# Optimization experiments

Hardware: AMD Instinct MI355X
Metric: run time of the kernel (lower is better)

Reference implementation:

```python
import jax, jax.numpy as jnp
import numpy as np

S, B, E, H = 2048, 2, 1024, 16
DH = E // H
SCALING = DH ** -0.5


def setup_inputs() -> dict:
    key = jax.random.key(0)
    ks = jax.random.split(key, 9)
    std = 1.0 / np.sqrt(E)
    return {
        "query": jax.random.normal(ks[0], (S, B, E), jnp.float32),
        "wq": jax.random.normal(ks[1], (E, E), jnp.float32) * std,
        "bq": jax.random.normal(ks[2], (E,), jnp.float32) * 0.02,
        "wk": jax.random.normal(ks[3], (E, E), jnp.float32) * std,
        "bk": jax.random.normal(ks[4], (E,), jnp.float32) * 0.02,
        "wv": jax.random.normal(ks[5], (E, E), jnp.float32) * std,
        "bv": jax.random.normal(ks[6], (E,), jnp.float32) * 0.02,
        "wo": jax.random.normal(ks[7], (E, E), jnp.float32) * std,
        "bo": jax.random.normal(ks[8], (E,), jnp.float32) * 0.02,
    }


def reference(query, wq, bq, wk, bk, wv, bv, wo, bo):
    # query: [S, B, E] (time, batch, channel), self-attention: key=value=query
    q = (query @ wq.T + bq) * SCALING          # fairseq scales q, not scores
    k = query @ wk.T + bk
    v = query @ wv.T + bv
    # split heads: [S, B, H, DH]
    q = q.reshape(S, B, H, DH)
    k = k.reshape(S, B, H, DH)
    v = v.reshape(S, B, H, DH)
    scores = jnp.einsum("qbhd,kbhd->bhqk", q, k)   # [B, H, S, S]
    probs = jax.nn.softmax(scores, axis=-1)
    ctx = jnp.einsum("bhqk,kbhd->qbhd", probs, v)  # [S, B, H, DH]
    ctx = ctx.reshape(S, B, E)
    return ctx @ wo.T + bo                          # [S, B, E]
```

## Files before the change

kernel.cpp:

```cpp
#include <hip/hip_runtime.h>
#include <hip/hip_bf16.h>
#include <stdint.h>

#define S_LEN 2048
#define BATCH 2
#define EMB   1024
#define NH    16
#define DHEAD 64
#define ROWS  (S_LEN*BATCH)
#define SCALE_Q 0.125f

typedef __attribute__((ext_vector_type(8))) short bf16x8;
typedef __attribute__((ext_vector_type(4))) float f32x4;

typedef const __attribute__((address_space(1))) void* gas_ptr;
typedef __attribute__((address_space(3))) void* las_ptr;
#define GLD16(g, l) __builtin_amdgcn_global_load_lds((gas_ptr)(g), (las_ptr)(l), 16, 0, 0)

__device__ __forceinline__ unsigned short f2b(float f) {
  union { float f; unsigned int u; } v; v.f = f;
  unsigned int u = v.u;
  unsigned int r = (u + 0x7FFFu + ((u >> 16) & 1u)) >> 16;
  return (unsigned short)r;
}

__device__ __forceinline__ void cvt8(const float* __restrict__ s,
                                     unsigned short* __restrict__ d, size_t i) {
  float4 a = *reinterpret_cast<const float4*>(s + i);
  float4 b = *reinterpret_cast<const float4*>(s + i + 4);
  uint4 o;
  o.x = (unsigned)f2b(a.x) | ((unsigned)f2b(a.y) << 16);
  o.y = (unsigned)f2b(a.z) | ((unsigned)f2b(a.w) << 16);
  o.z = (unsigned)f2b(b.x) | ((unsigned)f2b(b.y) << 16);
  o.w = (unsigned)f2b(b.z) | ((unsigned)f2b(b.w) << 16);
  *reinterpret_cast<uint4*>(d + i) = o;
}

__global__ __launch_bounds__(256) void cvt_kernel(const float* __restrict__ s,
                                                  unsigned short* __restrict__ d) {
  size_t i = ((size_t)blockIdx.x * 256 + threadIdx.x) * 8;
  cvt8(s, d, i);
}

__global__ __launch_bounds__(256) void cvt4_kernel(
    const float* __restrict__ s0, const float* __restrict__ s1,
    const float* __restrict__ s2, const float* __restrict__ s3,
    unsigned short* __restrict__ d0, unsigned short* __restrict__ d1,
    unsigned short* __restrict__ d2, unsigned short* __restrict__ d3) {
  const float* s; unsigned short* d;
  switch (blockIdx.y) {
    case 0:  s = s0; d = d0; break;
    case 1:  s = s1; d = d1; break;
    case 2:  s = s2; d = d2; break;
    default: s = s3; d = d3; break;
  }
  size_t i = ((size_t)blockIdx.x * 256 + threadIdx.x) * 8;
  cvt8(s, d, i);
}

__device__ __forceinline__ void gemm_mainloop(const unsigned short* __restrict__ A,
                                              const unsigned short* __restrict__ Bw,
                                              int m0, int n0, f32x4 acc[4][4]) {
  __shared__ unsigned short Abuf[128 * 32];
  __shared__ unsigned short Bbuf[128 * 32];
  const int t    = threadIdx.x;
  const int lane = t & 63;
  const int w    = t >> 6;
  const int wr   = w >> 1, wc = w & 1;
  const int lm   = lane & 15;
  const int lkb  = (lane >> 4) * 8;

  f32x4 zf = {0.0f, 0.0f, 0.0f, 0.0f};
#pragma unroll
  for (int i = 0; i < 4; ++i)
#pragma unroll
    for (int j = 0; j < 4; ++j) acc[i][j] = zf;

  for (int k0 = 0; k0 < EMB; k0 += 32) {
#pragma unroll
    for (int q = 0; q < 2; ++q) {
      int c = t + q * 256;
      int r = c >> 2, ci = c & 3;
      GLD16(A  + (size_t)(m0 + r) * EMB + k0 + ci * 8,
            (char*)Abuf + (size_t)(q * 256 + w * 64) * 16);
      GLD16(Bw + (size_t)(n0 + r) * EMB + k0 + ci * 8,
            (char*)Bbuf + (size_t)(q * 256 + w * 64) * 16);
    }
    __syncthreads();

    bf16x8 af[4], bfr[4];
#pragma unroll
    for (int i = 0; i < 4; ++i)
      af[i] = *reinterpret_cast<const bf16x8*>(&Abuf[(wr * 64 + i * 16 + lm) * 32 + lkb]);
#pragma unroll
    for (int j = 0; j < 4; ++j)
      bfr[j] = *reinterpret_cast<const bf16x8*>(&Bbuf[(wc * 64 + j * 16 + lm) * 32 + lkb]);
#pragma unroll
    for (int i = 0; i < 4; ++i)
#pragma unroll
      for (int j = 0; j < 4; ++j)
        acc[i][j] = __builtin_amdgcn_mfma_f32_16x16x32_bf16(af[i], bfr[j], acc[i][j], 0, 0, 0);
    __syncthreads();
  }
}

__global__ __launch_bounds__(256) void gemm_qkv_kernel(
    const unsigned short* __restrict__ X,
    const unsigned short* __restrict__ Wq, const unsigned short* __restrict__ Wk,
    const unsigned short* __restrict__ Wv,
    const float* __restrict__ bq, const float* __restrict__ bk, const float* __restrict__ bv,
    unsigned short* __restrict__ Qb, unsigned short* __restrict__ Kb,
    unsigned short* __restrict__ Vb) {
  const int m0 = blockIdx.x * 128;
  const int n0 = blockIdx.y * 128;
  const int z  = blockIdx.z;
  const unsigned short* Bw = (z == 0) ? Wq : (z == 1) ? Wk : Wv;
  const float* bias        = (z == 0) ? bq : (z == 1) ? bk : bv;
  unsigned short* Out      = (z == 0) ? Qb : (z == 1) ? Kb : Vb;
  const float scale        = (z == 0) ? SCALE_Q : 1.0f;

  f32x4 acc[4][4];
  gemm_mainloop(X, Bw, m0, n0, acc);

  const int lane = threadIdx.x & 63;
  const int w    = threadIdx.x >> 6;
  const int wr   = w >> 1, wc = w & 1;
  const int lm   = lane & 15, lq = lane >> 4;
#pragma unroll
  for (int j = 0; j < 4; ++j) {
    int col = n0 + wc * 64 + j * 16 + lm;
    int h = col >> 6, dd = col & 63;
    float bc = bias[col];
#pragma unroll
    for (int i = 0; i < 4; ++i) {
#pragma unroll
      for (int r = 0; r < 4; ++r) {
        int row = m0 + wr * 64 + i * 16 + lq * 4 + r;
        int s = row >> 1, b = row & 1;
        float v = (acc[i][j][r] + bc) * scale;
        Out[((size_t)(b * NH + h) * S_LEN + s) * DHEAD + dd] = f2b(v);
      }
    }
  }
}

__global__ __launch_bounds__(256) void gemm_out_kernel(
    const unsigned short* __restrict__ Ctx, const unsigned short* __restrict__ Wo,
    const float* __restrict__ bo, float* __restrict__ Out) {
  const int m0 = blockIdx.x * 128;
  const int n0 = blockIdx.y * 128;
  f32x4 acc[4][4];
  gemm_mainloop(Ctx, Wo, m0, n0, acc);

  const int lane = threadIdx.x & 63;
  const int w    = threadIdx.x >> 6;
  const int wr   = w >> 1, wc = w & 1;
  const int lm   = lane & 15, lq = lane >> 4;
#pragma unroll
  for (int j = 0; j < 4; ++j) {
    int col = n0 + wc * 64 + j * 16 + lm;
    float bc = bo[col];
#pragma unroll
    for (int i = 0; i < 4; ++i) {
#pragma unroll
      for (int r = 0; r < 4; ++r) {
        int row = m0 + wr * 64 + i * 16 + lq * 4 + r;
        Out[(size_t)row * EMB + col] = acc[i][j][r] + bc;
      }
    }
  }
}

__global__ __launch_bounds__(256) void transpose_v_kernel(
    const unsigned short* __restrict__ Vb, unsigned short* __restrict__ Vtg) {
  const int bh = blockIdx.x;
  const int kb = blockIdx.y * 64;
  const unsigned short* src = Vb + (size_t)bh * S_LEN * DHEAD;
  unsigned short* dst = Vtg + (size_t)bh * DHEAD * S_LEN;
  __shared__ unsigned short T[64][80];
  const int t = threadIdx.x;
#pragma unroll
  for (int q = 0; q < 2; ++q) {
    int c = t + q * 256;
    int r = c >> 3, j = (c & 7) * 8;
    bf16x8 v = *reinterpret_cast<const bf16x8*>(src + (size_t)(kb + r) * DHEAD + j);
    *reinterpret_cast<bf16x8*>(&T[r][j]) = v;
  }
  __syncthreads();
  int d = t >> 2, kvc = (t & 3) * 16;
  bf16x8 o0, o1;
#pragma unroll
  for (int e = 0; e < 8; ++e) o0[e] = (short)T[kvc + e][d];
#pragma unroll
  for (int e = 0; e < 8; ++e) o1[e] = (short)T[kvc + 8 + e][d];
  *reinterpret_cast<bf16x8*>(dst + (size_t)d * S_LEN + kb + kvc) = o0;
  *reinterpret_cast<bf16x8*>(dst + (size_t)d * S_LEN + kb + kvc + 8) = o1;
}

__global__ __launch_bounds__(512) void attn_kernel(
    const unsigned short* __restrict__ Qb, const unsigned short* __restrict__ Kb,
    const unsigned short* __restrict__ Vtg, unsigned short* __restrict__ Ctx) {
  const int bh = blockIdx.x;
  const int q0 = blockIdx.y * 128;
  const int t    = threadIdx.x;
  const int lane = t & 63;
  const int w    = t >> 6;
  const int lm   = lane & 15, lq = lane >> 4;
  const unsigned short* Q  = Qb  + (size_t)bh * S_LEN * DHEAD;
  const unsigned short* K  = Kb  + (size_t)bh * S_LEN * DHEAD;
  const unsigned short* Vt = Vtg + (size_t)bh * DHEAD * S_LEN;

  __shared__ unsigned short Kl[2][64 * 64];
  __shared__ unsigned short Vl[2][64 * 64];
  __shared__ unsigned short Pl[8][16 * 72];

  const int qw = q0 + w * 16;

  bf16x8 aq[2];
#pragma unroll
  for (int c = 0; c < 2; ++c)
    aq[c] = *reinterpret_cast<const bf16x8*>(
        Q + (size_t)(qw + lm) * DHEAD + c * 32 + lq * 8);

  f32x4 zf = {0.0f, 0.0f, 0.0f, 0.0f};
  f32x4 accO[4];
#pragma unroll
  for (int ni = 0; ni < 4; ++ni) accO[ni] = zf;
  float m_s = -1e30f, l_s = 0.0f;

  auto STAGE = [&](int b, int kb) {
    int r = t >> 3, p = t & 7;
    int lc = p ^ (r & 7);
    GLD16(K  + (size_t)(kb + r) * DHEAD + lc * 8,
          (char*)&Kl[b][0] + (size_t)(w * 64) * 16);
    GLD16(Vt + (size_t)r * S_LEN + kb + lc * 8,
          (char*)&Vl[b][0] + (size_t)(w * 64) * 16);
  };

  STAGE(0, 0);
  asm volatile("s_waitcnt vmcnt(0)" ::: "memory");
  __syncthreads();

  int cur = 0;
  const int NT = S_LEN / 64;
  for (int it = 0; it < NT; ++it) {
    if (it + 1 < NT) STAGE(cur ^ 1, (it + 1) * 64);

    f32x4 p4[4];
#pragma unroll
    for (int ji = 0; ji < 4; ++ji) {
      int rr = ji * 16 + lm;
      bf16x8 k0 = *reinterpret_cast<const bf16x8*>(
          &Kl[cur][rr * 64 + ((lq) ^ (rr & 7)) * 8]);
      bf16x8 k1 = *reinterpret_cast<const bf16x8*>(
          &Kl[cur][rr * 64 + ((4 + lq) ^ (rr & 7)) * 8]);
      f32x4 s0 = __builtin_amdgcn_mfma_f32_16x16x32_bf16(k0, aq[0], zf, 0, 0, 0);
      p4[ji]   = __builtin_amdgcn_mfma_f32_16x16x32_bf16(k1, aq[1], s0, 0, 0, 0);
    }

    float tm = p4[0][0];
#pragma unroll
    for (int ji = 0; ji < 4; ++ji)
#pragma unroll
      for (int r = 0; r < 4; ++r) tm = fmaxf(tm, p4[ji][r]);
    tm = fmaxf(tm, __shfl_xor(tm, 16));
    tm = fmaxf(tm, __shfl_xor(tm, 32));
    float mn = fmaxf(m_s, tm);
    float sc = __expf(m_s - mn);
    float ps = 0.0f;
#pragma unroll
    for (int ji = 0; ji < 4; ++ji)
#pragma unroll
      for (int r = 0; r < 4; ++r) {
        float e = __expf(p4[ji][r] - mn);
        p4[ji][r] = e;
        ps += e;
      }
    ps += __shfl_xor(ps, 16);
    ps += __shfl_xor(ps, 32);
    l_s = l_s * sc + ps;
    m_s = mn;

#pragma unroll
    for (int r = 0; r < 4; ++r) {
      float scr = __shfl(sc, lq * 4 + r);
#pragma unroll
      for (int ni = 0; ni < 4; ++ni) accO[ni][r] *= scr;
    }

    unsigned short* Pw = &Pl[w][0];
#pragma unroll
    for (int ji = 0; ji < 4; ++ji) {
      uint2 u;
      u.x = (unsigned)f2b(p4[ji][0]) | ((unsigned)f2b(p4[ji][1]) << 16);
      u.y = (unsigned)f2b(p4[ji][2]) | ((unsigned)f2b(p4[ji][3]) << 16);
      *reinterpret_cast<uint2*>(&Pw[lm * 72 + ji * 16 + lq * 4]) = u;
    }

    bf16x8 ap[2];
#pragma unroll
    for (int c = 0; c < 2; ++c)
      ap[c] = *reinterpret_cast<const bf16x8*>(&Pw[lm * 72 + c * 32 + lq * 8]);
#pragma unroll
    for (int ni = 0; ni < 4; ++ni) {
      int dd = ni * 16 + lm;
#pragma unroll
      for (int c = 0; c < 2; ++c) {
        bf16x8 bv = *reinterpret_cast<const bf16x8*>(
            &Vl[cur][dd * 64 + ((c * 4 + lq) ^ (dd & 7)) * 8]);
        accO[ni] = __builtin_amdgcn_mfma_f32_16x16x32_bf16(ap[c], bv, accO[ni], 0, 0, 0);
      }
    }

    asm volatile("s_waitcnt vmcnt(0)" ::: "memory");
    __syncthreads();
    cur ^= 1;
  }

  const int b = bh >> 4, h = bh & 15;
#pragma unroll
  for (int r = 0; r < 4; ++r) {
    float rl = 1.0f / __shfl(l_s, lq * 4 + r);
    int srow = qw + lq * 4 + r;
    size_t rowbase = ((size_t)srow * BATCH + b) * EMB + (size_t)h * 64;
#pragma unroll
    for (int ni = 0; ni < 4; ++ni)
      Ctx[rowbase + ni * 16 + lm] = f2b(accO[ni][r] * rl);
  }
}

extern "C" void kernel_launch(void* const* d_in, const int* in_sizes, int n_in,
                              void* d_out, int out_size, void* d_ws, size_t ws_size,
                              hipStream_t stream) {
  const float* query = (const float*)d_in[0];
  const float* wq = (const float*)d_in[1];
  const float* bq = (const float*)d_in[2];
  const float* wk = (const float*)d_in[3];
  const float* bk = (const float*)d_in[4];
  const float* wv = (const float*)d_in[5];
  const float* bv = (const float*)d_in[6];
  const float* wo = (const float*)d_in[7];
  const float* bo = (const float*)d_in[8];
  float* out = (float*)d_out;

  unsigned short* p = (unsigned short*)d_ws;
  unsigned short* Xbf = p;                        p += (size_t)ROWS * EMB;
  unsigned short* Wqb = p;                        p += (size_t)EMB * EMB;
  unsigned short* Wkb = p;                        p += (size_t)EMB * EMB;
  unsigned short* Wvb = p;                        p += (size_t)EMB * EMB;
  unsigned short* Wob = p;                        p += (size_t)EMB * EMB;
  unsigned short* Qb  = p;                        p += (size_t)ROWS * EMB;
  unsigned short* Kb  = p;                        p += (size_t)ROWS * EMB;
  unsigned short* Vb  = p;                        p += (size_t)ROWS * EMB;
  unsigned short* Ctx = p;                        p += (size_t)ROWS * EMB;
  unsigned short* Vtg = Xbf;

  cvt_kernel<<<ROWS * EMB / 8 / 256, 256, 0, stream>>>(query, Xbf);
  cvt4_kernel<<<dim3(EMB * EMB / 8 / 256, 4), 256, 0, stream>>>(
      wq, wk, wv, wo, Wqb, Wkb, Wvb, Wob);
  gemm_qkv_kernel<<<dim3(ROWS / 128, EMB / 128, 3), 256, 0, stream>>>(
      Xbf, Wqb, Wkb, Wvb, bq, bk, bv, Qb, Kb, Vb);
  transpose_v_kernel<<<dim3(BATCH * NH, S_LEN / 64), 256, 0, stream>>>(Vb, Vtg);
  attn_kernel<<<dim3(BATCH * NH, S_LEN / 128), 512, 0, stream>>>(Qb, Kb, Vtg, Ctx);
  gemm_out_kernel<<<dim3(ROWS / 128, EMB / 128), 256, 0, stream>>>(Ctx, Wob, bo, out);
}
```

Before: 228.2 us.

## Double-buffer GEMM K=64 tiles, defer softmax rescale, use exp2 and packed bf16 cvt

The GEMM mainloop now uses K=64 tiles with XOR-swizzled LDS and double buffering, so the next tile loads while MFMAs run. The attention kernel folds log2(e) into the Q scale and uses exp2f. It skips the running-max rescale unless the max grows past a threshold, adds s_setprio around MFMA blocks, and uses the hardware packed bf16 convert. These changes target load latency, LDS bank conflicts and VALU work in the softmax, at the cost of more LDS and some added numerical risk from the deferred rescale.

```diff
diff --git a/kernel.cpp b/kernel.cpp
--- a/kernel.cpp
+++ b/kernel.cpp
@@ -8,7 +8,8 @@
 #define NH    16
 #define DHEAD 64
 #define ROWS  (S_LEN*BATCH)
-#define SCALE_Q 0.125f
+#define SCALE_Q 0.18033688011112042f
+#define DEFER_THR 11.0f
 
 typedef __attribute__((ext_vector_type(8))) short bf16x8;
 typedef __attribute__((ext_vector_type(4))) float f32x4;
@@ -22,6 +23,12 @@
   unsigned int u = v.u;
   unsigned int r = (u + 0x7FFFu + ((u >> 16) & 1u)) >> 16;
   return (unsigned short)r;
+}
+
+__device__ __forceinline__ unsigned cvt_pk_bf16(float lo, float hi) {
+  unsigned r;
+  asm("v_cvt_pk_bf16_f32 %0, %1, %2" : "=v"(r) : "v"(lo), "v"(hi));
+  return r;
 }
 
 __device__ __forceinline__ void cvt8(const float* __restrict__ s,
@@ -61,14 +68,14 @@
 __device__ __forceinline__ void gemm_mainloop(const unsigned short* __restrict__ A,
                                               const unsigned short* __restrict__ Bw,
                                               int m0, int n0, f32x4 acc[4][4]) {
-  __shared__ unsigned short Abuf[128 * 32];
-  __shared__ unsigned short Bbuf[128 * 32];
+  __shared__ unsigned short Ab[2][128 * 64];
+  __shared__ unsigned short Bb[2][128 * 64];
   const int t    = threadIdx.x;
   const int lane = t & 63;
   const int w    = t >> 6;
   const int wr   = w >> 1, wc = w & 1;
   const int lm   = lane & 15;
-  const int lkb  = (lane >> 4) * 8;
+  const int lq   = lane >> 4;
 
   f32x4 zf = {0.0f, 0.0f, 0.0f, 0.0f};
 #pragma unroll
@@ -76,31 +83,53 @@
 #pragma unroll
     for (int j = 0; j < 4; ++j) acc[i][j] = zf;
 
-  for (int k0 = 0; k0 < EMB; k0 += 32) {
-#pragma unroll
-    for (int q = 0; q < 2; ++q) {
+  auto STAGE = [&](int b, int k0) {
+#pragma unroll
+    for (int q = 0; q < 4; ++q) {
       int c = t + q * 256;
-      int r = c >> 2, ci = c & 3;
-      GLD16(A  + (size_t)(m0 + r) * EMB + k0 + ci * 8,
-            (char*)Abuf + (size_t)(q * 256 + w * 64) * 16);
-      GLD16(Bw + (size_t)(n0 + r) * EMB + k0 + ci * 8,
-            (char*)Bbuf + (size_t)(q * 256 + w * 64) * 16);
-    }
+      int r = c >> 3, ci = c & 7;
+      int lc = ci ^ (r & 7);
+      GLD16(A  + (size_t)(m0 + r) * EMB + k0 + lc * 8,
+            (char*)&Ab[b][0] + (size_t)(q * 256 + w * 64) * 16);
+      GLD16(Bw + (size_t)(n0 + r) * EMB + k0 + lc * 8,
+            (char*)&Bb[b][0] + (size_t)(q * 256 + w * 64) * 16);
+    }
+  };
+
+  STAGE(0, 0);
+  asm volatile("s_waitcnt vmcnt(0)" ::: "memory");
+  __syncthreads();
+
+  int cur = 0;
+  const int NT = EMB / 64;
+  for (int it = 0; it < NT; ++it) {
+    if (it + 1 < NT) STAGE(cur ^ 1, (it + 1) * 64);
+
+#pragma unroll
+    for (int kk = 0; kk < 2; ++kk) {
+      bf16x8 af[4], bfr[4];
+#pragma unroll
+      for (int i = 0; i < 4; ++i) {
+        int ra = wr * 64 + i * 16 + lm;
+        af[i] = *reinterpret_cast<const bf16x8*>(
+            &Ab[cur][ra * 64 + ((kk * 4 + lq) ^ (ra & 7)) * 8]);
+      }
+#pragma unroll
+      for (int j = 0; j < 4; ++j) {
+        int rb = wc * 64 + j * 16 + lm;
+        bfr[j] = *reinterpret_cast<const bf16x8*>(
+            &Bb[cur][rb * 64 + ((kk * 4 + lq) ^ (rb & 7)) * 8]);
+      }
+#pragma unroll
+      for (int i = 0; i < 4; ++i)
+#pragma unroll
+        for (int j = 0; j < 4; ++j)
+          acc[i][j] = __builtin_amdgcn_mfma_f32_16x16x32_bf16(af[i], bfr[j], acc[i][j], 0, 0, 0);
+    }
+
+    asm volatile("s_waitcnt vmcnt(0)" ::: "memory");
     __syncthreads();
-
-    bf16x8 af[4], bfr[4];
-#pragma unroll
-    for (int i = 0; i < 4; ++i)
-      af[i] = *reinterpret_cast<const bf16x8*>(&Abuf[(wr * 64 + i * 16 + lm) * 32 + lkb]);
-#pragma unroll
-    for (int j = 0; j < 4; ++j)
-      bfr[j] = *reinterpret_cast<const bf16x8*>(&Bbuf[(wc * 64 + j * 16 + lm) * 32 + lkb]);
-#pragma unroll
-    for (int i = 0; i < 4; ++i)
-#pragma unroll
-      for (int j = 0; j < 4; ++j)
-        acc[i][j] = __builtin_amdgcn_mfma_f32_16x16x32_bf16(af[i], bfr[j], acc[i][j], 0, 0, 0);
-    __syncthreads();
+    cur ^= 1;
   }
 }
 
@@ -247,6 +276,7 @@
     if (it + 1 < NT) STAGE(cur ^ 1, (it + 1) * 64);
 
     f32x4 p4[4];
+    __builtin_amdgcn_s_setprio(1);
 #pragma unroll
     for (int ji = 0; ji < 4; ++ji) {
       int rr = ji * 16 + lm;
@@ -257,43 +287,48 @@
       f32x4 s0 = __builtin_amdgcn_mfma_f32_16x16x32_bf16(k0, aq[0], zf, 0, 0, 0);
       p4[ji]   = __builtin_amdgcn_mfma_f32_16x16x32_bf16(k1, aq[1], s0, 0, 0, 0);
     }
-
-    float tm = p4[0][0];
-#pragma unroll
-    for (int ji = 0; ji < 4; ++ji)
-#pragma unroll
-      for (int r = 0; r < 4; ++r) tm = fmaxf(tm, p4[ji][r]);
+    __builtin_amdgcn_s_setprio(0);
+
+    float t0 = fmaxf(fmaxf(p4[0][0], p4[0][1]), fmaxf(p4[0][2], p4[0][3]));
+    float t1 = fmaxf(fmaxf(p4[1][0], p4[1][1]), fmaxf(p4[1][2], p4[1][3]));
+    float t2 = fmaxf(fmaxf(p4[2][0], p4[2][1]), fmaxf(p4[2][2], p4[2][3]));
+    float t3 = fmaxf(fmaxf(p4[3][0], p4[3][1]), fmaxf(p4[3][2], p4[3][3]));
+    float tm = fmaxf(fmaxf(t0, t1), fmaxf(t2, t3));
     tm = fmaxf(tm, __shfl_xor(tm, 16));
     tm = fmaxf(tm, __shfl_xor(tm, 32));
-    float mn = fmaxf(m_s, tm);
-    float sc = __expf(m_s - mn);
+
+    if (!__all(tm - m_s <= DEFER_THR)) {
+      float mn = fmaxf(m_s, tm);
+      float sc = exp2f(m_s - mn);
+      l_s *= sc;
+      m_s = mn;
+#pragma unroll
+      for (int r = 0; r < 4; ++r) {
+        float scr = __shfl(sc, lq * 4 + r);
+#pragma unroll
+        for (int ni = 0; ni < 4; ++ni) accO[ni][r] *= scr;
+      }
+    }
+
     float ps = 0.0f;
 #pragma unroll
     for (int ji = 0; ji < 4; ++ji)
 #pragma unroll
       for (int r = 0; r < 4; ++r) {
-        float e = __expf(p4[ji][r] - mn);
+        float e = exp2f(p4[ji][r] - m_s);
         p4[ji][r] = e;
         ps += e;
       }
     ps += __shfl_xor(ps, 16);
     ps += __shfl_xor(ps, 32);
-    l_s = l_s * sc + ps;
-    m_s = mn;
-
-#pragma unroll
-    for (int r = 0; r < 4; ++r) {
-      float scr = __shfl(sc, lq * 4 + r);
-#pragma unroll
-      for (int ni = 0; ni < 4; ++ni) accO[ni][r] *= scr;
-    }
+    l_s += ps;
 
     unsigned short* Pw = &Pl[w][0];
 #pragma unroll
     for (int ji = 0; ji < 4; ++ji) {
       uint2 u;
-      u.x = (unsigned)f2b(p4[ji][0]) | ((unsigned)f2b(p4[ji][1]) << 16);
-      u.y = (unsigned)f2b(p4[ji][2]) | ((unsigned)f2b(p4[ji][3]) << 16);
+      u.x = cvt_pk_bf16(p4[ji][0], p4[ji][1]);
+      u.y = cvt_pk_bf16(p4[ji][2], p4[ji][3]);
       *reinterpret_cast<uint2*>(&Pw[lm * 72 + ji * 16 + lq * 4]) = u;
     }
 
@@ -301,6 +336,7 @@
 #pragma unroll
     for (int c = 0; c < 2; ++c)
       ap[c] = *reinterpret_cast<const bf16x8*>(&Pw[lm * 72 + c * 32 + lq * 8]);
+    __builtin_amdgcn_s_setprio(1);
 #pragma unroll
     for (int ni = 0; ni < 4; ++ni) {
       int dd = ni * 16 + lm;
@@ -311,6 +347,7 @@
         accO[ni] = __builtin_amdgcn_mfma_f32_16x16x32_bf16(ap[c], bv, accO[ni], 0, 0, 0);
       }
     }
+    __builtin_amdgcn_s_setprio(0);
 
     asm volatile("s_waitcnt vmcnt(0)" ::: "memory");
     __syncthreads();
```

Measured after the change: 222.6 us. -2.5%, faster.
